# Optimization experiments

Hardware: AMD Instinct MI355X
Metric: run time of the kernel (lower is better)

## Reference

```python
import jax, jax.numpy as jnp
import numpy as np

B, S, D, H = 2, 2048, 2048, 16
HD = D // H  # head_dim = 128

def _rope_tables(head_dim, context_length, theta_base=10000.0):
    inv_freq = 1.0 / theta_base ** (jnp.arange(0, head_dim, 2, dtype=jnp.float32) / head_dim)
    pos = jnp.arange(context_length, dtype=jnp.float32)
    angles = pos[:, None] * inv_freq[None, :]            # [S, HD/2]
    angles = jnp.concatenate([angles, angles], axis=1)   # [S, HD]
    return jnp.cos(angles), jnp.sin(angles)

def _apply_rope(x, cos, sin):
    # x: [b, h, s, hd]; cos/sin: [s, hd]
    hd = x.shape[-1]
    x1, x2 = x[..., : hd // 2], x[..., hd // 2 :]
    rotated = jnp.concatenate([-x2, x1], axis=-1)
    return x * cos[None, None] + rotated * sin[None, None]

def setup_inputs() -> dict:
    key = jax.random.key(0)
    ks = jax.random.split(key, 5)
    x = jax.random.normal(ks[0], (B, S, D), dtype=jnp.float32)
    scale = 1.0 / np.sqrt(D)
    Wq = jax.random.normal(ks[1], (D, D), dtype=jnp.float32) * scale
    Wk = jax.random.normal(ks[2], (D, D), dtype=jnp.float32) * scale
    Wv = jax.random.normal(ks[3], (D, D), dtype=jnp.float32) * scale
    Wo = jax.random.normal(ks[4], (D, D), dtype=jnp.float32) * scale
    cos, sin = _rope_tables(HD, S)
    return {"x": x, "Wq": Wq, "Wk": Wk, "Wv": Wv, "Wo": Wo, "cos": cos, "sin": sin}

def reference(x, Wq, Wk, Wv, Wo, cos, sin):
    b, s, _ = x.shape
    def split_heads(t):  # [b,s,D] -> [b,H,s,HD]
        return t.reshape(b, s, H, HD).transpose(0, 2, 1, 3)
    q = split_heads(x @ Wq.T)
    k = split_heads(x @ Wk.T)
    v = split_heads(x @ Wv.T)
    q = _apply_rope(q, cos[:s], sin[:s])
    k = _apply_rope(k, cos[:s], sin[:s])
    scores = jnp.einsum("bhqd,bhkd->bhqk", q, k) / np.sqrt(HD)
    causal = jnp.triu(jnp.ones((s, s), dtype=bool), k=1)
    scores = jnp.where(causal[None, None], -jnp.inf, scores)
    weights = jax.nn.softmax(scores, axis=-1)
    ctx = jnp.einsum("bhqk,bhkd->bhqd", weights, v)
    ctx = ctx.transpose(0, 2, 1, 3).reshape(b, s, D)
    return ctx @ Wo.T
```

## Files before the change

### kernel.cpp

```cpp
#include <hip/hip_runtime.h>
#include <cstdint>
#include <cmath>

#define B_ 2
#define S_ 2048
#define D_ 2048
#define H_ 16
#define HD_ 128

#define NEG_SENTINEL -1.0e30f

typedef __bf16 bf16;
typedef __attribute__((ext_vector_type(4))) __bf16 bf16x4;
typedef __attribute__((ext_vector_type(8))) __bf16 bf16x8;
typedef __attribute__((ext_vector_type(4))) float f32x4;

__device__ __forceinline__ void gload_lds16(const void* g, void* l) {
  __builtin_amdgcn_global_load_lds(
      (const __attribute__((address_space(1))) unsigned int*)g,
      (__attribute__((address_space(3))) unsigned int*)l, 16, 0, 0);
}

__device__ __forceinline__ f32x4 mfma16(bf16x8 a, bf16x8 b, f32x4 c) {
  return __builtin_amdgcn_mfma_f32_16x16x32_bf16(a, b, c, 0, 0, 0);
}

__global__ __launch_bounds__(256) void cvt_f32_bf16(
    const float* __restrict__ in, bf16* __restrict__ out)
{
  int i = blockIdx.x * 256 + threadIdx.x;
  f32x4 v = ((const f32x4*)in)[i];
  bf16x4 o;
#pragma unroll
  for (int j = 0; j < 4; ++j) o[j] = (bf16)v[j];
  ((bf16x4*)out)[i] = o;
}

__global__ __launch_bounds__(256) void cvt_qkvx(
    const float* __restrict__ x, bf16* __restrict__ xb,
    const float* __restrict__ wq, const float* __restrict__ wk,
    const float* __restrict__ wv, bf16* __restrict__ wout)
{
  int b = (int)blockIdx.x;
  const float* in; bf16* out; int base;
  if (b < 8192)      { in = x;  out = xb; base = b; }
  else {
    int r = b - 8192; int j = r >> 12; base = r & 4095;
    if (j == 0)      { in = wq; out = wout; }
    else if (j == 1) { in = wk; out = wout + 4194304; }
    else             { in = wv; out = wout + 8388608; }
  }
  int i = base * 256 + threadIdx.x;
  f32x4 v = ((const f32x4*)in)[i];
  bf16x4 o;
#pragma unroll
  for (int t2 = 0; t2 < 4; ++t2) o[t2] = (bf16)v[t2];
  ((bf16x4*)out)[i] = o;
}

#define GTM 128
#define GTN 128
#define GBK 64

template <typename OT>
__global__ __launch_bounds__(256) void gemm_xwt(
    const bf16* __restrict__ A, const bf16* __restrict__ W, OT* __restrict__ C,
    int M, int N, int K, int ldc)
{
  __shared__ bf16 sA[GTM * GBK];
  __shared__ bf16 sB[GTN * GBK];
  const int tid  = threadIdx.x;
  const int wave = tid >> 6, lane = tid & 63;
  const int quad = lane >> 4, l16 = lane & 15;
  const int tm = blockIdx.y * GTM;
  const int tn = blockIdx.x * GTN;
  const int wm = (wave >> 1) * 64, wn = (wave & 1) * 64;

  f32x4 acc[4][4];
#pragma unroll
  for (int i = 0; i < 4; ++i)
#pragma unroll
    for (int j = 0; j < 4; ++j) acc[i][j] = (f32x4)0.0f;

  for (int k0 = 0; k0 < K; k0 += GBK) {
    __syncthreads();
#pragma unroll
    for (int g = 0; g < 4; ++g) {
      int gb  = (g * 4 + wave) * 64;
      int p   = gb + lane;
      int row = p >> 3, pos = p & 7;
      int cc  = pos ^ (row & 7);
      gload_lds16(A + (size_t)(tm + row) * K + k0 + cc * 8, (char*)sA + (size_t)gb * 16);
      gload_lds16(W + (size_t)(tn + row) * K + k0 + cc * 8, (char*)sB + (size_t)gb * 16);
    }
    __syncthreads();

#pragma unroll
    for (int t = 0; t < 2; ++t) {
      bf16x8 af[4], bfr[4];
#pragma unroll
      for (int i = 0; i < 4; ++i) {
        int rowa = wm + i * 16 + l16;
        int posa = (t * 4 + quad) ^ (rowa & 7);
        af[i] = *(const bf16x8*)(sA + rowa * GBK + posa * 8);
        int rowb = wn + i * 16 + l16;
        int posb = (t * 4 + quad) ^ (rowb & 7);
        bfr[i] = *(const bf16x8*)(sB + rowb * GBK + posb * 8);
      }
#pragma unroll
      for (int i = 0; i < 4; ++i)
#pragma unroll
        for (int j = 0; j < 4; ++j)
          acc[i][j] = mfma16(af[i], bfr[j], acc[i][j]);
    }
  }

#pragma unroll
  for (int i = 0; i < 4; ++i)
#pragma unroll
    for (int r = 0; r < 4; ++r) {
      int row = tm + wm + i * 16 + quad * 4 + r;
#pragma unroll
      for (int j = 0; j < 4; ++j) {
        int col = tn + wn + j * 16 + l16;
        C[(size_t)row * ldc + col] = (OT)acc[i][j][r];
      }
    }
}

__global__ __launch_bounds__(256) void rope_qk(
    bf16* __restrict__ Q, bf16* __restrict__ Kk,
    const float* __restrict__ cosT, const float* __restrict__ sinT, int rs)
{
  const float kappa = 0.08838834764831845f * 1.4426950408889634f;
  int t = blockIdx.x * 256 + threadIdx.x;
  int d = t & 63;
  int h = (t >> 6) & (H_ - 1);
  int s = (t >> 10) & (S_ - 1);
  int b = t >> 21;
  size_t base = ((size_t)(b * S_ + s)) * rs + (size_t)h * HD_;
  float c1 = cosT[s * HD_ + d];
  float s1 = sinT[s * HD_ + d];
  float c2 = cosT[s * HD_ + d + 64];
  float s2 = sinT[s * HD_ + d + 64];
  {
    float x1 = (float)Q[base + d], x2 = (float)Q[base + d + 64];
    Q[base + d]      = (bf16)((x1 * c1 - x2 * s1) * kappa);
    Q[base + d + 64] = (bf16)((x2 * c2 + x1 * s2) * kappa);
  }
  {
    float x1 = (float)Kk[base + d], x2 = (float)Kk[base + d + 64];
    Kk[base + d]      = (bf16)(x1 * c1 - x2 * s1);
    Kk[base + d + 64] = (bf16)(x2 * c2 + x1 * s2);
  }
}

__global__ __launch_bounds__(256) void transpose_v(
    const bf16* __restrict__ V, bf16* __restrict__ Vt, int rs)
{
  __shared__ bf16 sT[64 * 72];
  const int tid = threadIdx.x;
  const int si = blockIdx.x;
  const int di = blockIdx.y;
  const int bh = blockIdx.z;
  const int b  = bh >> 4, h = bh & 15;

  const bf16* src = V + (size_t)b * S_ * rs + (size_t)h * HD_ + di * 64;
  bf16*       dst = Vt + ((size_t)bh * HD_ + di * 64) * S_ + si * 64;

#pragma unroll
  for (int half = 0; half < 2; ++half) {
    int r  = half * 32 + (tid >> 3);
    int c0 = (tid & 7) * 8;
    bf16x8 v = *(const bf16x8*)(src + (size_t)(si * 64 + r) * rs + c0);
    *(bf16x8*)(sT + r * 72 + c0) = v;
  }
  __syncthreads();
#pragma unroll
  for (int half = 0; half < 2; ++half) {
    int dr = half * 32 + (tid >> 3);
    int c0 = (tid & 7) * 8;
    bf16x8 o;
#pragma unroll
    for (int j = 0; j < 8; ++j) o[j] = sT[(c0 + j) * 72 + dr];
    *(bf16x8*)(dst + (size_t)dr * S_ + c0) = o;
  }
}

#define ABK 64
#define SPS 72

__global__ __launch_bounds__(256) void attn_fwd(
    const bf16* __restrict__ Q, const bf16* __restrict__ K,
    const bf16* __restrict__ Vt, bf16* __restrict__ O, int rs)
{
  __shared__ bf16 sK[ABK * HD_];
  __shared__ bf16 sVT[HD_ * ABK];
  __shared__ bf16 sP[64 * SPS];

  const int tid  = threadIdx.x;
  const int wave = tid >> 6, lane = tid & 63;
  const int quad = lane >> 4, l16 = lane & 15;

  const int lin   = (int)blockIdx.x;
  const int low3  = lin & 7;
  const int rest  = lin >> 3;
  const int qt    = 31 - (rest & 31);
  const int colhi = rest >> 5;
  const int col   = low3 + (colhi << 3);
  const int b = col >> 4, h = col & 15;

  const bf16* Qh  = Q + (size_t)b * S_ * rs + (size_t)h * HD_;
  const bf16* Kh  = K + (size_t)b * S_ * rs + (size_t)h * HD_;
  const bf16* Vth = Vt + ((size_t)(b * H_ + h) * HD_) * S_;
  bf16*       Oh  = O + (size_t)b * S_ * D_ + (size_t)h * HD_;

  const int wq = wave * 16;
  const int q0 = qt * 64;
  const int wq_abs = q0 + wq;

  bf16x8 qf[4];
  {
    const bf16* rp = Qh + (size_t)(wq_abs + l16) * rs + quad * 8;
#pragma unroll
    for (int t = 0; t < 4; ++t) qf[t] = *(const bf16x8*)(rp + t * 32);
  }

  f32x4 o_acc[8];
#pragma unroll
  for (int j = 0; j < 8; ++j) o_acc[j] = (f32x4)0.0f;
  float m_col = NEG_SENTINEL;
  float l_col = 0.0f;

  const int nkt = qt + 1;
#pragma unroll 1
  for (int kt = 0; kt < nkt; ++kt) {
    const int kk0 = kt * ABK;
    __syncthreads();

#pragma unroll
    for (int g = 0; g < 4; ++g) {
      int p   = g * 256 + tid;
      int row = p >> 4, pos = p & 15;
      int cc  = pos ^ (row & 15);
      gload_lds16(Kh + (size_t)(kk0 + row) * rs + cc * 8, (char*)sK + (size_t)p * 16);
    }
#pragma unroll
    for (int g = 0; g < 4; ++g) {
      int p  = g * 256 + tid;
      int d  = p >> 3, pos = p & 7;
      int cc = pos ^ (d & 7);
      gload_lds16(Vth + (size_t)d * S_ + kk0 + cc * 8, (char*)sVT + (size_t)p * 16);
    }
    __syncthreads();

    if (kk0 <= wq_abs + 15) {
      f32x4 st[4];
#pragma unroll
      for (int jt = 0; jt < 4; ++jt) {
        bf16x8 kf[4];
#pragma unroll
        for (int t = 0; t < 4; ++t) {
          int pos = (t * 4 + quad) ^ l16;
          kf[t] = *(const bf16x8*)(sK + (jt * 16 + l16) * HD_ + pos * 8);
        }
        f32x4 a2 = (f32x4)0.0f;
#pragma unroll
        for (int t = 0; t < 4; ++t) a2 = mfma16(kf[t], qf[t], a2);
        st[jt] = a2;
      }

      if (kk0 + 63 > wq_abs) {
        int qcol = wq_abs + l16;
#pragma unroll
        for (int jt = 0; jt < 4; ++jt)
#pragma unroll
          for (int r = 0; r < 4; ++r) {
            int key = kk0 + jt * 16 + quad * 4 + r;
            if (key > qcol) st[jt][r] = NEG_SENTINEL;
          }
      }

      float mx = NEG_SENTINEL;
#pragma unroll
      for (int jt = 0; jt < 4; ++jt)
#pragma unroll
        for (int r = 0; r < 4; ++r) mx = fmaxf(mx, st[jt][r]);
      mx = fmaxf(mx, __shfl_xor(mx, 16, 64));
      mx = fmaxf(mx, __shfl_xor(mx, 32, 64));
      float m_new = fmaxf(m_col, mx);
      float alpha = exp2f(m_col - m_new);
      float ts = 0.0f;
#pragma unroll
      for (int jt = 0; jt < 4; ++jt) {
        bf16x4 pk;
#pragma unroll
        for (int r = 0; r < 4; ++r) {
          float p = exp2f(st[jt][r] - m_new);
          ts += p;
          pk[r] = (bf16)p;
        }
        *(bf16x4*)(sP + (wq + l16) * SPS + jt * 16 + quad * 4) = pk;
      }
      ts += __shfl_xor(ts, 16, 64);
      ts += __shfl_xor(ts, 32, 64);
      l_col = l_col * alpha + ts;
      m_col = m_new;
#pragma unroll
      for (int r = 0; r < 4; ++r) {
        float av = __shfl(alpha, quad * 4 + r, 64);
#pragma unroll
        for (int jd = 0; jd < 8; ++jd) o_acc[jd][r] *= av;
      }

#pragma unroll
      for (int ks = 0; ks < 2; ++ks) {
        bf16x8 pf = *(const bf16x8*)(sP + (wq + l16) * SPS + ks * 32 + quad * 8);
#pragma unroll
        for (int jd = 0; jd < 8; ++jd) {
          int pos = (ks * 4 + quad) ^ (l16 & 7);
          bf16x8 vf = *(const bf16x8*)(sVT + (jd * 16 + l16) * ABK + pos * 8);
          o_acc[jd] = mfma16(pf, vf, o_acc[jd]);
        }
      }
    }
  }

#pragma unroll
  for (int r = 0; r < 4; ++r) {
    float lv = __shfl(l_col, quad * 4 + r, 64);
    float inv_l = 1.0f / lv;
    int row = wq_abs + quad * 4 + r;
#pragma unroll
    for (int jd = 0; jd < 8; ++jd) {
      int colo = jd * 16 + l16;
      Oh[(size_t)row * D_ + colo] = (bf16)(o_acc[jd][r] * inv_l);
    }
  }
}

extern "C" void kernel_launch(void* const* d_in, const int* in_sizes, int n_in,
                              void* d_out, int out_size, void* d_ws, size_t ws_size,
                              hipStream_t stream) {
  const float* x    = (const float*)d_in[0];
  const float* Wq   = (const float*)d_in[1];
  const float* Wk   = (const float*)d_in[2];
  const float* Wv   = (const float*)d_in[3];
  const float* Wo   = (const float*)d_in[4];
  const float* cosT = (const float*)d_in[5];
  const float* sinT = (const float*)d_in[6];
  float* out = (float*)d_out;

  const size_t NE = (size_t)B_ * S_ * D_;
  const size_t WE = (size_t)D_ * D_;
  const int M = B_ * S_;
  const int cvtX = (int)(NE / 1024);
  const int cvtW = (int)(WE / 1024);

  if (ws_size >= (size_t)92274688) {
    bf16* QKV   = (bf16*)d_ws;
    bf16* xb    = QKV + (size_t)M * 6144;
    bf16* Wqkv  = xb + NE;
    bf16* ctx   = Wqkv;
    bf16* Wob   = Wqkv + 2 * WE;
    bf16* Vt    = xb;

    cvt_qkvx<<<8192 + 3 * 4096, 256, 0, stream>>>(x, xb, Wq, Wk, Wv, Wqkv);
    gemm_xwt<bf16><<<dim3(48, 32), 256, 0, stream>>>(xb, Wqkv, QKV, M, 3 * D_, D_, 3 * D_);
    rope_qk<<<(B_ * S_ * H_ * 64) / 256, 256, 0, stream>>>(QKV, QKV + D_, cosT, sinT, 3 * D_);
    transpose_v<<<dim3(32, 2, 32), 256, 0, stream>>>(QKV + 2 * D_, Vt, 3 * D_);
    attn_fwd<<<1024, 256, 0, stream>>>(QKV, QKV + D_, Vt, ctx, 3 * D_);
    cvt_f32_bf16<<<cvtW, 256, 0, stream>>>(Wo, Wob);
    gemm_xwt<float><<<dim3(16, 32), 256, 0, stream>>>(ctx, Wob, out, M, D_, D_, D_);
  } else {
    bf16* Qb    = (bf16*)d_ws;
    bf16* Kb    = Qb + NE;
    bf16* Vb    = Kb + NE;
    bf16* Cb    = Vb + NE;
    bf16* Wslot = Cb + NE;

    cvt_f32_bf16<<<cvtX, 256, 0, stream>>>(x, Cb);
    cvt_f32_bf16<<<cvtW, 256, 0, stream>>>(Wq, Wslot);
    gemm_xwt<bf16><<<dim3(16, 32), 256, 0, stream>>>(Cb, Wslot, Qb, M, D_, D_, D_);
    cvt_f32_bf16<<<cvtW, 256, 0, stream>>>(Wk, Wslot);
    gemm_xwt<bf16><<<dim3(16, 32), 256, 0, stream>>>(Cb, Wslot, Kb, M, D_, D_, D_);
    cvt_f32_bf16<<<cvtW, 256, 0, stream>>>(Wv, Wslot);
    gemm_xwt<bf16><<<dim3(16, 32), 256, 0, stream>>>(Cb, Wslot, Vb, M, D_, D_, D_);
    rope_qk<<<(B_ * S_ * H_ * 64) / 256, 256, 0, stream>>>(Qb, Kb, cosT, sinT, D_);
    transpose_v<<<dim3(32, 2, 32), 256, 0, stream>>>(Vb, Cb, D_);
    attn_fwd<<<1024, 256, 0, stream>>>(Qb, Kb, Cb, Vb, D_);
    cvt_f32_bf16<<<cvtW, 256, 0, stream>>>(Wo, Wslot);
    gemm_xwt<float><<<dim3(16, 32), 256, 0, stream>>>(Vb, Wslot, out, M, D_, D_, D_);
  }
}
```

Measured before the change: 414.6 us.

## Double attention query tile to 128 rows with 8 waves; vectorize RoPE

The attention kernel now runs 8 waves per block over a 128-row query tile, so each K/V tile staged in LDS is reused by twice as many query rows. This halves K/V global traffic, at the cost of fewer, larger blocks and coarser causal load balance. The RoPE kernel is also rewritten so each thread handles 8 contiguous elements with 16-byte vector loads and stores, replacing scalar accesses. Hidden sections (the sP indexing and the per-wave mask logic) must scale to 128 rows for the change to be correct.

```diff
diff --git a/kernel.cpp b/kernel.cpp
--- a/kernel.cpp
+++ b/kernel.cpp
@@ -133,26 +133,37 @@
     const float* __restrict__ cosT, const float* __restrict__ sinT, int rs)
 {
   const float kappa = 0.08838834764831845f * 1.4426950408889634f;
-  int t = blockIdx.x * 256 + threadIdx.x;
-  int d = t & 63;
-  int h = (t >> 6) & (H_ - 1);
-  int s = (t >> 10) & (S_ - 1);
-  int b = t >> 21;
+  int t  = blockIdx.x * 256 + threadIdx.x;
+  int d0 = (t & 7) * 8;
+  int h  = (t >> 3) & (H_ - 1);
+  int s  = (t >> 7) & (S_ - 1);
+  int b  = t >> 18;
   size_t base = ((size_t)(b * S_ + s)) * rs + (size_t)h * HD_;
-  float c1 = cosT[s * HD_ + d];
-  float s1 = sinT[s * HD_ + d];
-  float c2 = cosT[s * HD_ + d + 64];
-  float s2 = sinT[s * HD_ + d + 64];
-  {
-    float x1 = (float)Q[base + d], x2 = (float)Q[base + d + 64];
-    Q[base + d]      = (bf16)((x1 * c1 - x2 * s1) * kappa);
-    Q[base + d + 64] = (bf16)((x2 * c2 + x1 * s2) * kappa);
-  }
-  {
-    float x1 = (float)Kk[base + d], x2 = (float)Kk[base + d + 64];
-    Kk[base + d]      = (bf16)(x1 * c1 - x2 * s1);
-    Kk[base + d + 64] = (bf16)(x2 * c2 + x1 * s2);
-  }
+
+  const float* cl = cosT + s * HD_ + d0;
+  const float* sl = sinT + s * HD_ + d0;
+
+  bf16x8 ql = *(const bf16x8*)(Q + base + d0);
+  bf16x8 qh = *(const bf16x8*)(Q + base + 64 + d0);
+  bf16x8 kl = *(const bf16x8*)(Kk + base + d0);
+  bf16x8 kh = *(const bf16x8*)(Kk + base + 64 + d0);
+
+  bf16x8 qlo, qho, klo, kho;
+#pragma unroll
+  for (int i = 0; i < 8; ++i) {
+    float c1 = cl[i], s1 = sl[i];
+    float c2 = cl[64 + i], s2 = sl[64 + i];
+    float x1 = (float)ql[i], x2 = (float)qh[i];
+    qlo[i] = (bf16)((x1 * c1 - x2 * s1) * kappa);
+    qho[i] = (bf16)((x2 * c2 + x1 * s2) * kappa);
+    float y1 = (float)kl[i], y2 = (float)kh[i];
+    klo[i] = (bf16)(y1 * c1 - y2 * s1);
+    kho[i] = (bf16)(y2 * c2 + y1 * s2);
+  }
+  *(bf16x8*)(Q + base + d0)       = qlo;
+  *(bf16x8*)(Q + base + 64 + d0)  = qho;
+  *(bf16x8*)(Kk + base + d0)      = klo;
+  *(bf16x8*)(Kk + base + 64 + d0) = kho;
 }
 
 __global__ __launch_bounds__(256) void transpose_v(
@@ -190,13 +201,13 @@
 #define ABK 64
 #define SPS 72
 
-__global__ __launch_bounds__(256) void attn_fwd(
+__global__ __launch_bounds__(512) void attn_fwd(
     const bf16* __restrict__ Q, const bf16* __restrict__ K,
     const bf16* __restrict__ Vt, bf16* __restrict__ O, int rs)
 {
   __shared__ bf16 sK[ABK * HD_];
   __shared__ bf16 sVT[HD_ * ABK];
-  __shared__ bf16 sP[64 * SPS];
+  __shared__ bf16 sP[128 * SPS];
 
   const int tid  = threadIdx.x;
   const int wave = tid >> 6, lane = tid & 63;
@@ -205,8 +216,8 @@
   const int lin   = (int)blockIdx.x;
   const int low3  = lin & 7;
   const int rest  = lin >> 3;
-  const int qt    = 31 - (rest & 31);
-  const int colhi = rest >> 5;
+  const int qt    = 15 - (rest & 15);
+  const int colhi = rest >> 4;
   const int col   = low3 + (colhi << 3);
   const int b = col >> 4, h = col & 15;
 
@@ -216,7 +227,7 @@
   bf16*       Oh  = O + (size_t)b * S_ * D_ + (size_t)h * HD_;
 
   const int wq = wave * 16;
-  const int q0 = qt * 64;
+  const int q0 = qt * 128;
   const int wq_abs = q0 + wq;
 
   bf16x8 qf[4];
@@ -232,22 +243,22 @@
   float m_col = NEG_SENTINEL;
   float l_col = 0.0f;
 
-  const int nkt = qt + 1;
+  const int nkt = 2 * qt + 2;
 #pragma unroll 1
   for (int kt = 0; kt < nkt; ++kt) {
     const int kk0 = kt * ABK;
     __syncthreads();
 
 #pragma unroll
-    for (int g = 0; g < 4; ++g) {
-      int p   = g * 256 + tid;
+    for (int g = 0; g < 2; ++g) {
+      int p   = g * 512 + tid;
       int row = p >> 4, pos = p & 15;
       int cc  = pos ^ (row & 15);
       gload_lds16(Kh + (size_t)(kk0 + row) * rs + cc * 8, (char*)sK + (size_t)p * 16);
     }
 #pragma unroll
-    for (int g = 0; g < 4; ++g) {
-      int p  = g * 256 + tid;
+    for (int g = 0; g < 2; ++g) {
+      int p  = g * 512 + tid;
       int d  = p >> 3, pos = p & 7;
       int cc = pos ^ (d & 7);
       gload_lds16(Vth + (size_t)d * S_ + kk0 + cc * 8, (char*)sVT + (size_t)p * 16);
@@ -356,6 +367,7 @@
   const int M = B_ * S_;
   const int cvtX = (int)(NE / 1024);
   const int cvtW = (int)(WE / 1024);
+  const int ropeG = (B_ * S_ * H_ * 8) / 256;
 
   if (ws_size >= (size_t)92274688) {
     bf16* QKV   = (bf16*)d_ws;
@@ -367,9 +379,9 @@
 
     cvt_qkvx<<<8192 + 3 * 4096, 256, 0, stream>>>(x, xb, Wq, Wk, Wv, Wqkv);
     gemm_xwt<bf16><<<dim3(48, 32), 256, 0, stream>>>(xb, Wqkv, QKV, M, 3 * D_, D_, 3 * D_);
-    rope_qk<<<(B_ * S_ * H_ * 64) / 256, 256, 0, stream>>>(QKV, QKV + D_, cosT, sinT, 3 * D_);
+    rope_qk<<<ropeG, 256, 0, stream>>>(QKV, QKV + D_, cosT, sinT, 3 * D_);
     transpose_v<<<dim3(32, 2, 32), 256, 0, stream>>>(QKV + 2 * D_, Vt, 3 * D_);
-    attn_fwd<<<1024, 256, 0, stream>>>(QKV, QKV + D_, Vt, ctx, 3 * D_);
+    attn_fwd<<<512, 512, 0, stream>>>(QKV, QKV + D_, Vt, ctx, 3 * D_);
     cvt_f32_bf16<<<cvtW, 256, 0, stream>>>(Wo, Wob);
     gemm_xwt<float><<<dim3(16, 32), 256, 0, stream>>>(ctx, Wob, out, M, D_, D_, D_);
   } else {
@@ -386,9 +398,9 @@
     gemm_xwt<bf16><<<dim3(16, 32), 256, 0, stream>>>(Cb, Wslot, Kb, M, D_, D_, D_);
     cvt_f32_bf16<<<cvtW, 256, 0, stream>>>(Wv, Wslot);
     gemm_xwt<bf16><<<dim3(16, 32), 256, 0, stream>>>(Cb, Wslot, Vb, M, D_, D_, D_);
-    rope_qk<<<(B_ * S_ * H_ * 64) / 256, 256, 0, stream>>>(Qb, Kb, cosT, sinT, D_);
+    rope_qk<<<ropeG, 256, 0, stream>>>(Qb, Kb, cosT, sinT, D_);
     transpose_v<<<dim3(32, 2, 32), 256, 0, stream>>>(Vb, Cb, D_);
-    attn_fwd<<<1024, 256, 0, stream>>>(Qb, Kb, Cb, Vb, D_);
+    attn_fwd<<<512, 512, 0, stream>>>(Qb, Kb, Cb, Vb, D_);
     cvt_f32_bf16<<<cvtW, 256, 0, stream>>>(Wo, Wslot);
     gemm_xwt<float><<<dim3(16, 32), 256, 0, stream>>>(Vb, Wslot, out, M, D_, D_, D_);
   }
```

New measurement: 408.5 us. Within noise of the previous version (-1.5%).
